# Performance work log

Hardware: AMD Instinct MI355X
Metric: run time of the kernel (lower is better)

The kernel has to match this reference:

```python
import jax, jax.numpy as jnp
import numpy as np

EPS = 1e-8
LN_EPS = 1e-5
DIM, NHEADS = 512, 8
HEAD_DIM = DIM // NHEADS
SCALE = HEAD_DIM ** -0.5
ROLE_VOCAB = 8


def _layernorm(x, g, b):
    mu = x.mean(-1, keepdims=True)
    var = ((x - mu) ** 2).mean(-1, keepdims=True)
    return (x - mu) * jax.lax.rsqrt(var + LN_EPS) * g + b


def setup_inputs() -> dict:
    key = jax.random.key(0)
    ks = jax.random.split(key, 16)
    B, K, L, D = 8, 4, 1024, DIM
    s = 1.0 / np.sqrt(D)
    return {
        "state_repr": jax.random.normal(ks[0], (B, K, L, D), jnp.float32),
        "residue_mask": jax.random.randint(ks[1], (B, K, L), 0, 2) > 0,
        "state_weights": jax.random.uniform(ks[2], (B, K), jnp.float32),
        "state_roles": jax.random.randint(ks[3], (B, K), 0, ROLE_VOCAB),
        "state_present_mask": jnp.ones((B, K), dtype=bool),
        "role_emb": jax.random.normal(ks[4], (ROLE_VOCAB, D), jnp.float32),
        "Wq": jax.random.normal(ks[5], (D, D), jnp.float32) * s,
        "Wk": jax.random.normal(ks[6], (D, D), jnp.float32) * s,
        "Wv": jax.random.normal(ks[7], (D, D), jnp.float32) * s,
        "Wo": jax.random.normal(ks[8], (D, D), jnp.float32) * s,
        "ln1_g": jnp.ones((3 * D,), jnp.float32),
        "ln1_b": jnp.zeros((3 * D,), jnp.float32),
        "Wg1": jax.random.normal(ks[9], (D, 3 * D), jnp.float32) / np.sqrt(3 * D),
        "bg1": jnp.zeros((D,), jnp.float32),
        "Wg2": jax.random.normal(ks[10], (D, D), jnp.float32) * s,
        "bg2": jnp.zeros((D,), jnp.float32),
        "norm_g": jnp.ones((D,), jnp.float32),
        "norm_b": jnp.zeros((D,), jnp.float32),
    }


def _forward(state_repr, residue_mask, state_weights, state_roles, state_present_mask,
             role_emb, Wq, Wk, Wv, Wo, ln1_g, ln1_b, Wg1, bg1, Wg2, bg2, norm_g, norm_b):
    B, K, L, D = state_repr.shape
    H, hd = NHEADS, HEAD_DIM
    roles = jnp.maximum(state_roles, 0)
    role_e = role_emb[roles][:, :, None, :]                       # [B,K,1,D]
    valid = residue_mask & state_present_mask[:, :, None]          # [B,K,L]

    # normalized state weights
    pres = state_present_mask.astype(jnp.float32)
    w = state_weights.astype(jnp.float32) * pres
    denom = w.sum(1, keepdims=True)
    fallback = pres / jnp.maximum(pres.sum(1, keepdims=True), 1.0)
    nsw = jnp.where(denom > EPS, w / jnp.maximum(denom, EPS), fallback)  # [B,K]

    x = (state_repr + role_e) * valid[..., None]
    x = x.transpose(0, 2, 1, 3)                                    # [B,L,K,D]
    valid_rlk = valid.transpose(0, 2, 1)                           # [B,L,K]

    def proj(W):  # torch Linear: y = x @ W.T
        return (x @ W.T).reshape(B, L, K, H, hd).transpose(0, 1, 3, 2, 4)  # [B,L,H,K,hd]

    q, k, v = proj(Wq), proj(Wk), proj(Wv)
    logits = jnp.einsum('blhqd,blhkd->blhqk', q, k) * SCALE
    logits = logits + jnp.log(jnp.maximum(nsw, EPS))[:, None, None, None, :]
    key_mask = valid_rlk[:, :, None, None, :]                      # [B,L,1,1,K]
    logits = jnp.where(key_mask, logits, -jnp.inf)
    attn = jax.nn.softmax(logits, axis=-1)
    attn = jnp.nan_to_num(attn, nan=0.0, posinf=0.0, neginf=0.0)
    attn_out = jnp.einsum('blhqk,blhkd->blhqd', attn, v)
    attn_out = attn_out.transpose(0, 1, 3, 2, 4).reshape(B, L, K, D)
    attn_out = (attn_out @ Wo.T) * valid_rlk[..., None]

    swr = nsw[:, None, :] * valid_rlk.astype(jnp.float32)          # [B,L,K]
    swr = swr / jnp.maximum(swr.sum(-1, keepdims=True), EPS)
    weighted_mean = jnp.sum(x * swr[..., None], axis=2)            # [B,L,D]
    attn_pooled = jnp.sum(attn_out * swr[..., None], axis=2)

    max_in = jnp.where(valid_rlk[..., None], x, -1e9)
    max_feat = max_in.max(axis=2)
    has_any = valid_rlk.any(axis=2, keepdims=True)
    max_feat = jnp.where(has_any, max_feat, 0.0)

    fusion_base = 0.5 * (attn_pooled + weighted_mean)
    gate_in = jnp.concatenate([attn_pooled, weighted_mean, max_feat], axis=-1)
    h = _layernorm(gate_in, ln1_g, ln1_b)
    h = jax.nn.gelu(h @ Wg1.T + bg1, approximate=False)
    gate = jax.nn.sigmoid(h @ Wg2.T + bg2)
    fused = gate * fusion_base + (1.0 - gate) * max_feat
    fused = _layernorm(fused + weighted_mean, norm_g, norm_b)

    attn_mean = attn.mean(axis=(2, 3))                             # [B,L,K]
    return fused, attn_pooled, weighted_mean, max_feat, attn_mean, nsw


def reference(state_repr, residue_mask, state_weights, state_roles, state_present_mask,
              role_emb, Wq, Wk, Wv, Wo, ln1_g, ln1_b, Wg1, bg1, Wg2, bg2, norm_g, norm_b):
    return _forward(state_repr, residue_mask, state_weights, state_roles, state_present_mask,
                    role_emb, Wq, Wk, Wv, Wo, ln1_g, ln1_b, Wg1, bg1, Wg2, bg2, norm_g, norm_b)
```

## Files before the change

kernel.cpp:

```cpp
#include <hip/hip_runtime.h>
#include <math.h>

#define BB 8
#define KK 4
#define LL 1024
#define DD 512
#define HD 64
#define D3 1536
#define MM (BB*LL*KK)
#define BL (BB*LL)
#define SCALE 0.125f
#define EPSF 1e-8f
#define LN_EPSF 1e-5f

typedef _Float16 hfrag __attribute__((ext_vector_type(8)));
typedef float f32x4 __attribute__((ext_vector_type(4)));

__device__ __forceinline__ unsigned short f2h(float f) {
    _Float16 h = (_Float16)f;
    unsigned short u; __builtin_memcpy(&u, &h, 2); return u;
}
__device__ __forceinline__ float h2f(unsigned short u) {
    _Float16 h; __builtin_memcpy(&h, &u, 2); return (float)h;
}

__device__ __forceinline__ void glds16(const unsigned short* g, unsigned short* l) {
    __builtin_amdgcn_global_load_lds(
        (const __attribute__((address_space(1))) void*)g,
        (__attribute__((address_space(3))) void*)l, 16, 0, 0);
}

__device__ __forceinline__ void nsw_compute(const float* sw, const int* pres,
                                            int b, float* nswv) {
    float w[KK], pr[KK]; float denom = 0.f, ps = 0.f;
    #pragma unroll
    for (int k = 0; k < KK; ++k) {
        pr[k] = pres[b*KK + k] ? 1.f : 0.f;
        w[k]  = sw[b*KK + k] * pr[k];
        denom += w[k]; ps += pr[k];
    }
    #pragma unroll
    for (int k = 0; k < KK; ++k)
        nswv[k] = (denom > EPSF) ? w[k] / fmaxf(denom, EPSF)
                                 : pr[k] / fmaxf(ps, 1.f);
}

#define WSZ 262144
#define OG1 1048576
#define OG2 1835008
#define WTOT 2097152
__global__ __launch_bounds__(256) void cvt_weights(
        const float* __restrict__ Wq, const float* __restrict__ Wk,
        const float* __restrict__ Wv, const float* __restrict__ Wo,
        const float* __restrict__ Wg1, const float* __restrict__ Wg2,
        unsigned short* __restrict__ dst) {
    int t = blockIdx.x * 256 + threadIdx.x;
    int e = t * 4;
    const float* src; int off;
    if      (e < WSZ)    { src = Wq;  off = e; }
    else if (e < 2*WSZ)  { src = Wk;  off = e - WSZ; }
    else if (e < 3*WSZ)  { src = Wv;  off = e - 2*WSZ; }
    else if (e < OG1)    { src = Wo;  off = e - 3*WSZ; }
    else if (e < OG2)    { src = Wg1; off = e - OG1; }
    else                 { src = Wg2; off = e - OG2; }
    float4 v = *(const float4*)(src + off);
    ushort4 o;
    o.x = f2h(v.x); o.y = f2h(v.y); o.z = f2h(v.z); o.w = f2h(v.w);
    *(ushort4*)(dst + e) = o;
}

__global__ __launch_bounds__(256) void buildx_kernel(
        const float* __restrict__ SR, const int* __restrict__ residue,
        const int* __restrict__ pres, const int* __restrict__ roles,
        const float* __restrict__ role_emb, const float* __restrict__ sw,
        unsigned short* __restrict__ Xh, float* __restrict__ rowmask,
        float* __restrict__ out_wm, float* __restrict__ out_mx,
        float* __restrict__ f_nsw) {
    int t  = blockIdx.x * 256 + threadIdx.x;
    int bl = t >> 7;
    int d4 = (t & 127) << 2;
    int b  = bl >> 10, l = bl & 1023;
    float nswv[KK];
    nsw_compute(sw, pres, b, nswv);
    float mk[KK], swr[KK];
    float ssum = 0.f, many = 0.f;
    #pragma unroll
    for (int k = 0; k < KK; ++k) {
        int bk = b*KK + k;
        bool valid = (residue[(size_t)bk*LL + l] != 0) && (pres[bk] != 0);
        mk[k]  = valid ? 1.f : 0.f;
        swr[k] = nswv[k] * mk[k];
        ssum += swr[k]; many += mk[k];
    }
    float inv = 1.f / fmaxf(ssum, EPSF);
    bool hasany = many > 0.5f;
    float wmx = 0.f, wmy = 0.f, wmz = 0.f, wmw = 0.f;
    float mxx = -1e9f, mxy = -1e9f, mxz = -1e9f, mxw = -1e9f;
    #pragma unroll
    for (int k = 0; k < KK; ++k) {
        int bk = b*KK + k;
        int role = roles[bk]; if (role < 0) role = 0;
        float4 sr = *(const float4*)(SR + ((size_t)bk*LL + l)*DD + d4);
        float4 re = *(const float4*)(role_emb + (size_t)role*DD + d4);
        float xx = (sr.x + re.x)*mk[k], xy = (sr.y + re.y)*mk[k];
        float xz = (sr.z + re.z)*mk[k], xw = (sr.w + re.w)*mk[k];
        ushort4 xs; xs.x = f2h(xx); xs.y = f2h(xy); xs.z = f2h(xz); xs.w = f2h(xw);
        *(ushort4*)(Xh + (size_t)(bl*KK + k)*DD + d4) = xs;
        float s = swr[k]*inv;
        wmx = fmaf(xx, s, wmx); wmy = fmaf(xy, s, wmy);
        wmz = fmaf(xz, s, wmz); wmw = fmaf(xw, s, wmw);
        if (mk[k] > 0.5f) {
            mxx = fmaxf(mxx, xx); mxy = fmaxf(mxy, xy);
            mxz = fmaxf(mxz, xz); mxw = fmaxf(mxw, xw);
        }
    }
    if (!hasany) { mxx = mxy = mxz = mxw = 0.f; }
    float4 wmv; wmv.x = wmx; wmv.y = wmy; wmv.z = wmz; wmv.w = wmw;
    float4 mxv; mxv.x = mxx; mxv.y = mxy; mxv.z = mxz; mxv.w = mxw;
    *(float4*)(out_wm + (size_t)bl*DD + d4) = wmv;
    *(float4*)(out_mx + (size_t)bl*DD + d4) = mxv;
    if (d4 == 0) {
        #pragma unroll
        for (int k = 0; k < KK; ++k) rowmask[bl*KK + k] = mk[k];
    }
    if (blockIdx.x == 0 && threadIdx.x < BB*KK) {
        int bb = threadIdx.x >> 2, kk2 = threadIdx.x & 3;
        float nv[KK];
        nsw_compute(sw, pres, bb, nv);
        f_nsw[threadIdx.x] = nv[kk2];
    }
}

template<int TM, int EPI, int OUTH, int QKVR, int SWZ>
__global__ __launch_bounds__(256) void gemm_mfma(
        const unsigned short* __restrict__ A, const unsigned short* __restrict__ W,
        void* __restrict__ Cv, int M, int N, int Kd,
        const float* __restrict__ bias, const float* __restrict__ rowmask) {
    constexpr int FI = TM / 32;
    __shared__ __align__(16) unsigned short As[TM*32];
    __shared__ __align__(16) unsigned short Bs[128*32];
    const int tid  = threadIdx.x;
    const int wave = tid >> 6, lane = tid & 63;
    int m0, n0;
    if (SWZ) {
        int id = blockIdx.x;
        int c = id & 7, j = id >> 3;
        int mloc = j / 12;
        m0 = (c*32 + mloc) * TM;
        n0 = (j - mloc*12) * 128;
    } else {
        m0 = blockIdx.y * TM; n0 = blockIdx.x * 128;
    }
    const int srow = lane >> 2;
    const int scol = (lane & 3) << 3;
    const int arow = (TM == 128) ? (wave*32 + srow)
                   : (TM == 64)  ? (wave*16 + srow)
                   :               ((wave & 1)*16 + srow);
    const bool astage = (TM >= 64) || (wave < 2);
    const unsigned short* Ag0 = A + (size_t)(m0 + arow) * Kd + scol;
    const unsigned short* Ag1 = Ag0 + (size_t)16 * Kd;
    unsigned short* Al0 = As + arow*32 + scol;
    unsigned short* Al1 = Al0 + 16*32;
    const unsigned short* Wp0 = W + (size_t)(n0 + wave*32 + srow) * Kd + scol;
    const unsigned short* Wp1 = Wp0 + (size_t)16 * Kd;
    unsigned short* Bl0 = Bs + (wave*32 + srow)*32 + scol;
    unsigned short* Bl1 = Bl0 + 16*32;
    const int wr = (wave >> 1) * (TM/2);
    const int wc = (wave & 1) * 64;
    const int fr = lane & 15;
    const int fq = (lane >> 4) * 8;
    f32x4 acc[FI][4] = {};
    for (int k0 = 0; k0 < Kd; k0 += 32) {
        if (astage)    glds16(Ag0 + k0, Al0);
        if (TM == 128) glds16(Ag1 + k0, Al1);
        glds16(Wp0 + k0, Bl0);
        glds16(Wp1 + k0, Bl1);
        __syncthreads();
        hfrag af[FI], bf[4];
        #pragma unroll
        for (int i = 0; i < FI; ++i)
            af[i] = *(const hfrag*)(As + (wr + i*16 + fr)*32 + fq);
        #pragma unroll
        for (int j = 0; j < 4; ++j)
            bf[j] = *(const hfrag*)(Bs + (wc + j*16 + fr)*32 + fq);
        #pragma unroll
        for (int i = 0; i < FI; ++i)
            #pragma unroll
            for (int j = 0; j < 4; ++j)
                acc[i][j] = __builtin_amdgcn_mfma_f32_16x16x32_f16(af[i], bf[j], acc[i][j], 0, 0, 0);
        __syncthreads();
    }
    unsigned short* Ch = (unsigned short*)Cv;
    int Nout = N, colbase = n0;
    if (QKVR) {
        const int seg = n0 >> 9;
        Ch = (unsigned short*)Cv + (size_t)seg * M * 512;
        Nout = 512;
        colbase = n0 - (seg << 9);
    }
    #pragma unroll
    for (int i = 0; i < FI; ++i) {
        const int row = m0 + wr + i*16 + (lane >> 4)*4;
        #pragma unroll
        for (int j = 0; j < 4; ++j) {
            const int col = colbase + wc + j*16 + (lane & 15);
            float bv = (EPI == 2) ? bias[col] : 0.f;
            #pragma unroll
            for (int r = 0; r < 4; ++r) {
                float v = acc[i][j][r];
                if (EPI == 2) { v += bv; v = 0.5f * v * (1.f + erff(v * 0.70710678118654752f)); }
                if (OUTH) Ch[(size_t)(row + r) * Nout + col] = f2h(v);
                else      ((float*)Cv)[(size_t)(row + r) * Nout + col] = v;
            }
        }
    }
}

__global__ __launch_bounds__(512, 2) void gemm_qkv_8p(
        const unsigned short* __restrict__ A, const unsigned short* __restrict__ W,
        unsigned short* __restrict__ Cbase) {
    __shared__ __align__(16) unsigned short smem[65536];
    const int tid  = threadIdx.x;
    const int wave = tid >> 6, lane = tid & 63;
    const int id = blockIdx.x;
    const int wg = (id & 7) * 96 + (id >> 3);
    const int m0 = (wg / 6) * 256;
    const int n0 = (wg % 6) * 256;
    const int wm = wave >> 2, wn = wave & 3;
    const int fr = lane & 15, q = lane >> 4;
    const int c0 = (wave << 6) | lane;
    const int r0 = c0 >> 2, cc0 = c0 & 3;
    const int c1 = c0 + 512;
    const int r1 = c1 >> 2, cc1 = c1 & 3;
    const unsigned short* Ag0 = A + (size_t)(m0 + r0)*512 + ((cc0 ^ ((r0 >> 1) & 3)) << 3);
    const unsigned short* Ag1 = A + (size_t)(m0 + r1)*512 + ((cc1 ^ ((r1 >> 1) & 3)) << 3);
    const unsigned short* Wp0 = W + (size_t)(n0 + r0)*512 + ((cc0 ^ ((r0 >> 1) & 3)) << 3);
    const unsigned short* Wp1 = W + (size_t)(n0 + r1)*512 + ((cc1 ^ ((r1 >> 1) & 3)) << 3);
    const int lA0 = c0 << 3, lA1 = c1 << 3;
    int aoff[8], boff[4];
    #pragma unroll
    for (int mf = 0; mf < 8; ++mf) {
        int row = (wm << 7) + (mf << 4) + fr;
        aoff[mf] = (row << 5) + ((q ^ ((row >> 1) & 3)) << 3);
    }
    #pragma unroll
    for (int nf = 0; nf < 4; ++nf) {
        int row = (wn << 6) + (nf << 4) + fr;
        boff[nf] = (row << 5) + ((q ^ ((row >> 1) & 3)) << 3);
    }
    f32x4 acc[8][4] = {};

#define VMWAIT(N) asm volatile("s_waitcnt vmcnt(" #N ")" ::: "memory")
#define STAGE(tt) do { unsigned short* _d = smem + (((tt) & 3) << 14); \
        const int _ko = (tt) << 5; \
        glds16(Ag0 + _ko, _d + lA0); glds16(Ag1 + _ko, _d + lA1); \
        glds16(Wp0 + _ko, _d + 8192 + lA0); glds16(Wp1 + _ko, _d + 8192 + lA1); } while (0)
#define MFROW(ai, areg) \
        acc[ai][0] = __builtin_amdgcn_mfma_f32_16x16x32_f16(areg, b0, acc[ai][0], 0, 0, 0); \
        acc[ai][1] = __builtin_amdgcn_mfma_f32_16x16x32_f16(areg, b1, acc[ai][1], 0, 0, 0); \
        acc[ai][2] = __builtin_amdgcn_mfma_f32_16x16x32_f16(areg, b2, acc[ai][2], 0, 0, 0); \
        acc[ai][3] = __builtin_amdgcn_mfma_f32_16x16x32_f16(areg, b3, acc[ai][3], 0, 0, 0);
#define TILE(t, STG, VM) do { \
        const unsigned short* _Ab = smem + (((t) & 3) << 14); \
        const unsigned short* _Bb = _Ab + 8192; \
        VMWAIT(VM); \
        __builtin_amdgcn_s_barrier(); \
        __builtin_amdgcn_sched_barrier(0); \
        hfrag b0 = *(const hfrag*)(_Bb + boff[0]); \
        hfrag b1 = *(const hfrag*)(_Bb + boff[1]); \
        hfrag b2 = *(const hfrag*)(_Bb + boff[2]); \
        hfrag b3 = *(const hfrag*)(_Bb + boff[3]); \
        hfrag a0_ = *(const hfrag*)(_Ab + aoff[0]); \
        hfrag a1_ = *(const hfrag*)(_Ab + aoff[1]); \
        hfrag a2_ = *(const hfrag*)(_Ab + aoff[2]); \
        hfrag a3_ = *(const hfrag*)(_Ab + aoff[3]); \
        hfrag a4_ = *(const hfrag*)(_Ab + aoff[4]); \
        hfrag a5_ = *(const hfrag*)(_Ab + aoff[5]); \
        hfrag a6_ = *(const hfrag*)(_Ab + aoff[6]); \
        hfrag a7_ = *(const hfrag*)(_Ab + aoff[7]); \
        if (STG) STAGE((t) + 3); \
        __builtin_amdgcn_s_setprio(1); \
        MFROW(0, a0_) MFROW(1, a1_) MFROW(2, a2_) MFROW(3, a3_) \
        MFROW(4, a4_) MFROW(5, a5_) MFROW(6, a6_) MFROW(7, a7_) \
        __builtin_amdgcn_s_setprio(0); \
    } while (0)

    STAGE(0); STAGE(1); STAGE(2);
    for (int t = 0; t < 13; ++t) TILE(t, 1, 8);
    TILE(13, 0, 8);
    TILE(14, 0, 4);
    TILE(15, 0, 0);
#undef TILE
#undef MFROW
#undef STAGE
#undef VMWAIT

    const int gc0 = n0 + (wn << 6);
    const int seg = gc0 >> 9;
    unsigned short* Cs = Cbase + (size_t)seg * ((size_t)MM * 512);
    const int cb = gc0 & 511;
    #pragma unroll
    for (int mf = 0; mf < 8; ++mf) {
        const int grow = m0 + (wm << 7) + (mf << 4) + (q << 2);
        #pragma unroll
        for (int nf = 0; nf < 4; ++nf) {
            const int col = cb + (nf << 4) + fr;
            #pragma unroll
            for (int r = 0; r < 4; ++r)
                Cs[(size_t)(grow + r) * 512 + col] = f2h(acc[mf][nf][r]);
        }
    }
}

__global__ __launch_bounds__(256) void wo_pool_kernel(
        const unsigned short* __restrict__ A,
        const unsigned short* __restrict__ W,
        const float* __restrict__ sw, const int* __restrict__ pres,
        const float* __restrict__ rmask,
        const float* __restrict__ in_wm, const float* __restrict__ in_mx,
        const float* __restrict__ ln1_g, const float* __restrict__ ln1_b,
        float* __restrict__ out_ap, unsigned short* __restrict__ hin) {
    __shared__ __align__(16) unsigned short As[32*32];
    __shared__ __align__(16) unsigned short Bs[512*32];
    const int tid = threadIdx.x, wave = tid >> 6, lane = tid & 63;
    const int m0 = blockIdx.x * 32;
    const int srow = lane >> 2, scol = (lane & 3) << 3;
    const unsigned short* Ag = A + (size_t)(m0 + wave*16 + srow)*512 + scol;
    unsigned short* Al = As + (wave*16 + srow)*32 + scol;
    const int brow = wave*128 + srow;
    const unsigned short* Wg = W + (size_t)brow*512 + scol;
    unsigned short* Blb = Bs + brow*32 + scol;
    const int q = lane >> 4, frl = lane & 15;
    const int fq = q * 8;
    f32x4 acc[2][8] = {};
    for (int k0 = 0; k0 < 512; k0 += 32) {
        if (wave < 2) glds16(Ag + k0, Al);
        #pragma unroll
        for (int i = 0; i < 8; ++i)
            glds16(Wg + (size_t)i*16*512 + k0, Blb + i*16*32);
        __syncthreads();
        hfrag af[2], bf[8];
        #pragma unroll
        for (int i = 0; i < 2; ++i)
            af[i] = *(const hfrag*)(As + (i*16 + frl)*32 + fq);
        #pragma unroll
        for (int j = 0; j < 8; ++j)
            bf[j] = *(const hfrag*)(Bs + (wave*128 + j*16 + frl)*32 + fq);
        #pragma unroll
        for (int i = 0; i < 2; ++i)
            #pragma unroll
            for (int j = 0; j < 8; ++j)
                acc[i][j] = __builtin_amdgcn_mfma_f32_16x16x32_f16(af[i], bf[j], acc[i][j], 0, 0, 0);
        __syncthreads();
    }
    float* ap_s = (float*)Bs;
    const int bl0 = m0 >> 2;
    const int b = bl0 >> 10;
    float nv[KK];
    nsw_compute(sw, pres, b, nv);
    #pragma unroll
    for (int i = 0; i < 2; ++i) {
        int bl_loc = i*4 + q;
        int blg = bl0 + bl_loc;
        float s4[KK]; float ssum = 0.f;
        #pragma unroll
        for (int k = 0; k < KK; ++k) { s4[k] = nv[k] * rmask[blg*4 + k]; ssum += s4[k]; }
        float inv = 1.f / fmaxf(ssum, EPSF);
        #pragma unroll
        for (int j = 0; j < 8; ++j) {
            float ap = 0.f;
            #pragma unroll
            for (int r = 0; r < KK; ++r) ap = fmaf(s4[r]*inv, acc[i][j][r], ap);
            ap_s[bl_loc*512 + wave*128 + j*16 + frl] = ap;
        }
    }
    __syncthreads();
    const int blq = tid >> 5;
    const int c0  = (tid & 31) * 16;
    const int blg = bl0 + blq;
    float4 ap4[4], wm4[4], mx4[4];
    #pragma unroll
    for (int v = 0; v < 4; ++v) {
        ap4[v] = *(const float4*)(ap_s + blq*512 + c0 + v*4);
        wm4[v] = *(const float4*)(in_wm + (size_t)blg*512 + c0 + v*4);
        mx4[v] = *(const float4*)(in_mx + (size_t)blg*512 + c0 + v*4);
    }
    float s = 0.f, s2 = 0.f;
    #pragma unroll
    for (int c = 0; c < 16; ++c) {
        float ap = ((const float*)ap4)[c];
        float wm = ((const float*)wm4)[c];
        float mx = ((const float*)mx4)[c];
        s += ap + wm + mx; s2 += ap*ap + wm*wm + mx*mx;
    }
    #pragma unroll
    for (int o = 1; o < 32; o <<= 1) {
        s  += __shfl_xor(s,  o, 32);
        s2 += __shfl_xor(s2, o, 32);
    }
    float mu = s * (1.f/(float)D3);
    float var = s2 * (1.f/(float)D3) - mu*mu;
    float rstd = rsqrtf(var + LN_EPSF);
    #pragma unroll
    for (int v = 0; v < 4; ++v)
        *(float4*)(out_ap + (size_t)blg*512 + c0 + v*4) = ap4[v];
    #pragma unroll
    for (int seg = 0; seg < 3; ++seg) {
        const float* src = (seg == 0) ? (const float*)ap4
                         : (seg == 1) ? (const float*)wm4 : (const float*)mx4;
        int gofs = seg*512 + c0;
        #pragma unroll
        for (int v = 0; v < 4; ++v) {
            float4 g4 = *(const float4*)(ln1_g + gofs + v*4);
            float4 b4 = *(const float4*)(ln1_b + gofs + v*4);
            ushort4 o;
            o.x = f2h((src[v*4+0]-mu)*rstd*g4.x + b4.x);
            o.y = f2h((src[v*4+1]-mu)*rstd*g4.y + b4.y);
            o.z = f2h((src[v*4+2]-mu)*rstd*g4.z + b4.z);
            o.w = f2h((src[v*4+3]-mu)*rstd*g4.w + b4.w);
            *(ushort4*)(hin + (size_t)blg*D3 + gofs + v*4) = o;
        }
    }
}

__global__ __launch_bounds__(256) void wg2_final_kernel(
        const unsigned short* __restrict__ A,
        const unsigned short* __restrict__ W,
        const float* __restrict__ bg2,
        const float* __restrict__ in_ap, const float* __restrict__ in_wm,
        const float* __restrict__ in_mx,
        const float* __restrict__ norm_g, const float* __restrict__ norm_b,
        float* __restrict__ fused) {
    __shared__ __align__(16) unsigned short As[16*32];
    __shared__ __align__(16) unsigned short Bs[512*32];
    __shared__ float rs[16*4], rq[16*4];
    const int tid = threadIdx.x, wave = tid >> 6, lane = tid & 63;
    const int m0 = blockIdx.x * 16;
    const int srow = lane >> 2, scol = (lane & 3) << 3;
    const unsigned short* Ag = A + (size_t)(m0 + srow)*512 + scol;
    unsigned short* Al = As + srow*32 + scol;
    const int brow = wave*128 + srow;
    const unsigned short* Wg = W + (size_t)brow*512 + scol;
    unsigned short* Blb = Bs + brow*32 + scol;
    const int q = lane >> 4, frl = lane & 15;
    const int fq = q * 8;
    f32x4 acc[8] = {};
    for (int k0 = 0; k0 < 512; k0 += 32) {
        if (wave == 0) glds16(Ag + k0, Al);
        #pragma unroll
        for (int i = 0; i < 8; ++i)
            glds16(Wg + (size_t)i*16*512 + k0, Blb + i*16*32);
        __syncthreads();
        hfrag af, bf[8];
        af = *(const hfrag*)(As + frl*32 + fq);
        #pragma unroll
        for (int j = 0; j < 8; ++j)
            bf[j] = *(const hfrag*)(Bs + (wave*128 + j*16 + frl)*32 + fq);
        #pragma unroll
        for (int j = 0; j < 8; ++j)
            acc[j] = __builtin_amdgcn_mfma_f32_16x16x32_f16(af, bf[j], acc[j], 0, 0, 0);
        __syncthreads();
    }
    float pre[8][4];
    float s[4] = {}, s2[4] = {};
    #pragma unroll
    for (int j = 0; j < 8; ++j) {
        int col = wave*128 + j*16 + frl;
        float bv = bg2[col];
        #pragma unroll
        for (int r = 0; r < 4; ++r) {
            int row = m0 + q*4 + r;
            float g = 1.f / (1.f + expf(-(acc[j][r] + bv)));
            float ap = in_ap[(size_t)row*512 + col];
            float wm = in_wm[(size_t)row*512 + col];
            float mx = in_mx[(size_t)row*512 + col];
            float p = g*0.5f*(ap + wm) + (1.f - g)*mx + wm;
            pre[j][r] = p;
            s[r] += p; s2[r] += p*p;
        }
    }
    #pragma unroll
    for (int r = 0; r < 4; ++r) {
        #pragma unroll
        for (int o = 1; o < 16; o <<= 1) {
            s[r]  += __shfl_xor(s[r],  o, 64);
            s2[r] += __shfl_xor(s2[r], o, 64);
        }
        if (frl == 0) {
            rs[(q*4+r)*4 + wave] = s[r];
            rq[(q*4+r)*4 + wave] = s2[r];
        }
    }
    __syncthreads();
    float mu[4], rstd[4];
    #pragma unroll
    for (int r = 0; r < 4; ++r) {
        int rl = q*4 + r;
        float ts  = rs[rl*4] + rs[rl*4+1] + rs[rl*4+2] + rs[rl*4+3];
        float tq  = rq[rl*4] + rq[rl*4+1] + rq[rl*4+2] + rq[rl*4+3];
        float m = ts * (1.f/(float)DD);
        float v = tq * (1.f/(float)DD) - m*m;
        mu[r] = m; rstd[r] = rsqrtf(v + LN_EPSF);
    }
    #pragma unroll
    for (int j = 0; j < 8; ++j) {
        int col = wave*128 + j*16 + frl;
        float g = norm_g[col], bb = norm_b[col];
        #pragma unroll
        for (int r = 0; r < 4; ++r) {
            int row = m0 + q*4 + r;
            fused[(size_t)row*512 + col] = (pre[j][r]-mu[r])*rstd[r]*g + bb;
        }
    }
}

__global__ __launch_bounds__(256) void attn_kernel(
        unsigned short* Qb ,
        const unsigned short* __restrict__ Kb, const unsigned short* __restrict__ Vb,
        const float* __restrict__ sw, const int* __restrict__ pres,
        const float* __restrict__ rowmask,
        float* __restrict__ attn_mean_out) {
    __shared__ float qs[KK][DD];
    __shared__ float ksm[KK][DD];
    __shared__ float vs[KK][DD];
    __shared__ float att[128];
    __shared__ float lw[KK], mk[KK];
    int bl = blockIdx.x, b = bl >> 10, mb = bl * KK;
    int tid = threadIdx.x;
    const ushort4* q4 = (const ushort4*)(Qb + (size_t)mb*DD);
    const ushort4* k4 = (const ushort4*)(Kb + (size_t)mb*DD);
    const ushort4* v4 = (const ushort4*)(Vb + (size_t)mb*DD);
    #pragma unroll
    for (int p = 0; p < 2; ++p) {
        int idx = p*256 + tid;
        int k = idx >> 7, dd = (idx & 127) << 2;
        ushort4 a = q4[idx];
        qs[k][dd] = h2f(a.x); qs[k][dd+1] = h2f(a.y); qs[k][dd+2] = h2f(a.z); qs[k][dd+3] = h2f(a.w);
        ushort4 c = k4[idx];
        ksm[k][dd] = h2f(c.x); ksm[k][dd+1] = h2f(c.y); ksm[k][dd+2] = h2f(c.z); ksm[k][dd+3] = h2f(c.w);
        ushort4 e = v4[idx];
        vs[k][dd] = h2f(e.x); vs[k][dd+1] = h2f(e.y); vs[k][dd+2] = h2f(e.z); vs[k][dd+3] = h2f(e.w);
    }
    if (tid < KK) {
        float nv[KK];
        nsw_compute(sw, pres, b, nv);
        lw[tid] = logf(fmaxf(nv[tid], EPSF));
        mk[tid] = rowmask[mb + tid];
    }
    __syncthreads();
    if (tid < 128) {
        int h = tid >> 4, i = (tid >> 2) & 3, j = tid & 3;
        float s = 0.f;
        #pragma unroll 16
        for (int d = 0; d < HD; ++d) s = fmaf(qs[i][h*HD + d], ksm[j][h*HD + d], s);
        float lg = s * SCALE + lw[j];
        att[tid] = (mk[j] > 0.5f) ? lg : -INFINITY;
    }
    __syncthreads();
    if (tid < 32) {
        int base = tid * 4;
        float l0 = att[base], l1 = att[base+1], l2 = att[base+2], l3 = att[base+3];
        float m = fmaxf(fmaxf(l0, l1), fmaxf(l2, l3));
        if (m == -INFINITY) {
            att[base] = att[base+1] = att[base+2] = att[base+3] = 0.f;
        } else {
            float e0 = expf(l0 - m), e1 = expf(l1 - m), e2 = expf(l2 - m), e3 = expf(l3 - m);
            float inv = 1.f / (e0 + e1 + e2 + e3);
            att[base] = e0*inv; att[base+1] = e1*inv; att[base+2] = e2*inv; att[base+3] = e3*inv;
        }
    }
    __syncthreads();
    if (tid < KK) {
        float s = 0.f;
        for (int hi = 0; hi < 32; ++hi) s += att[hi*4 + tid];
        attn_mean_out[(size_t)bl*KK + tid] = s * (1.f/32.f);
    }
    float outv[8];
    #pragma unroll
    for (int p = 0; p < 8; ++p) {
        int idx = p*256 + tid;
        int i = idx >> 9, dc = idx & 511, h = dc >> 6;
        float s = 0.f;
        #pragma unroll
        for (int j = 0; j < KK; ++j) s = fmaf(att[h*16 + i*4 + j], vs[j][dc], s);
        outv[p] = s;
    }
    #pragma unroll
    for (int p = 0; p < 8; ++p) {
        int idx = p*256 + tid;
        int i = idx >> 9, dc = idx & 511;
        Qb[(size_t)(mb+i)*DD + dc] = f2h(outv[p]);
    }
}

extern "C" void kernel_launch(void* const* d_in, const int* in_sizes, int n_in,
                              void* d_out, int out_size, void* d_ws, size_t ws_size,
                              hipStream_t stream) {
    const float* SR      = (const float*)d_in[0];
    const int*   residue = (const int*)d_in[1];
    const float* sw      = (const float*)d_in[2];
    const int*   roles   = (const int*)d_in[3];
    const int*   pres    = (const int*)d_in[4];
    const float* role_emb= (const float*)d_in[5];
    const float* Wq      = (const float*)d_in[6];
    const float* Wk      = (const float*)d_in[7];
    const float* Wv      = (const float*)d_in[8];
    const float* Wo      = (const float*)d_in[9];
    const float* ln1_g   = (const float*)d_in[10];
    const float* ln1_b   = (const float*)d_in[11];
    const float* Wg1     = (const float*)d_in[12];
    const float* bg1     = (const float*)d_in[13];
    const float* Wg2     = (const float*)d_in[14];
    const float* bg2     = (const float*)d_in[15];
    const float* norm_g  = (const float*)d_in[16];
    const float* norm_b  = (const float*)d_in[17];

    float* out = (float*)d_out;
    const size_t BLD = (size_t)BL * DD;
    float* f_fused = out;
    float* f_ap    = out + BLD;
    float* f_wm    = out + 2*BLD;
    float* f_mx    = out + 3*BLD;
    float* f_am    = out + 4*BLD;
    float* f_nsw   = out + 4*BLD + (size_t)BL*KK;

    char* base = (char*)d_ws;
    const size_t MD2 = (size_t)MM * DD * 2;
    unsigned short* Xh = (unsigned short*)(base);
    unsigned short* Qh = (unsigned short*)(base + MD2);
    unsigned short* Kh = (unsigned short*)(base + 2*MD2);
    unsigned short* Vh = (unsigned short*)(base + 3*MD2);
    unsigned short* Wb = (unsigned short*)(base + 4*MD2);
    float* rmask = (float*)(base + 4*MD2 + (size_t)WTOT*2);
    unsigned short* AOh  = Qh;
    unsigned short* Hin  = Vh;
    unsigned short* Hbuf = Xh;
    const unsigned short* Wqkv = Wb;
    const unsigned short* Woh  = Wb + 3*WSZ;
    const unsigned short* Wg1h = Wb + OG1;
    const unsigned short* Wg2h = Wb + OG2;

    dim3 blk(256);

    cvt_weights<<<WTOT/1024, blk, 0, stream>>>(Wq, Wk, Wv, Wo, Wg1, Wg2, Wb);
    buildx_kernel<<<(BL*128)/256, blk, 0, stream>>>(SR, residue, pres, roles, role_emb,
                                                    sw, Xh, rmask, f_wm, f_mx, f_nsw);

    gemm_qkv_8p<<<dim3(768), dim3(512), 0, stream>>>(Xh, Wqkv, Qh);

    attn_kernel<<<BL, blk, 0, stream>>>(Qh, Kh, Vh, sw, pres, rmask, f_am);

    wo_pool_kernel<<<dim3(MM/32), blk, 0, stream>>>(
        AOh, Woh, sw, pres, rmask, f_wm, f_mx, ln1_g, ln1_b, f_ap, Hin);

    gemm_mfma<32,2,1,0,0><<<dim3(4, BL/32), blk, 0, stream>>>(
        Hin, Wg1h, Hbuf, BL, DD, D3, bg1, nullptr);

    wg2_final_kernel<<<dim3(BL/16), blk, 0, stream>>>(
        Hbuf, Wg2h, bg2, f_ap, f_wm, f_mx, norm_g, norm_b, f_fused);
}
```

Baseline: 385.7 us.

## Shrink QKV GEMM tile to 256x128 with triple-buffered LDS for higher occupancy

The QKV projection GEMM tile goes from 256x256 to 256x128, with 8 waves arranged 4x2 and each wave holding a 64x64 accumulator. The LDS ring drops from four stages to three (72 KB) and the launch bound rises to 4 blocks per CU. The grid doubles to 1536 blocks. The goal is more resident waves and better latency hiding, at the cost of re-reading A more often and having less compute per loaded tile and a shallower prefetch.

```diff
diff --git a/kernel.cpp b/kernel.cpp
--- a/kernel.cpp
+++ b/kernel.cpp
@@ -216,31 +216,29 @@
     }
 }
 
-__global__ __launch_bounds__(512, 2) void gemm_qkv_8p(
+__global__ __launch_bounds__(512, 4) void gemm_qkv_8p(
         const unsigned short* __restrict__ A, const unsigned short* __restrict__ W,
         unsigned short* __restrict__ Cbase) {
-    __shared__ __align__(16) unsigned short smem[65536];
+    __shared__ __align__(16) unsigned short smem[36864];
     const int tid  = threadIdx.x;
     const int wave = tid >> 6, lane = tid & 63;
     const int id = blockIdx.x;
-    const int wg = (id & 7) * 96 + (id >> 3);
-    const int m0 = (wg / 6) * 256;
-    const int n0 = (wg % 6) * 256;
-    const int wm = wave >> 2, wn = wave & 3;
+    const int wg = (id & 7) * 192 + (id >> 3);
+    const int m0 = (wg / 12) * 256;
+    const int n0 = (wg % 12) * 128;
+    const int wm = wave >> 1, wn = wave & 1;
     const int fr = lane & 15, q = lane >> 4;
-    const int c0 = (wave << 6) | lane;
-    const int r0 = c0 >> 2, cc0 = c0 & 3;
-    const int c1 = c0 + 512;
-    const int r1 = c1 >> 2, cc1 = c1 & 3;
-    const unsigned short* Ag0 = A + (size_t)(m0 + r0)*512 + ((cc0 ^ ((r0 >> 1) & 3)) << 3);
-    const unsigned short* Ag1 = A + (size_t)(m0 + r1)*512 + ((cc1 ^ ((r1 >> 1) & 3)) << 3);
-    const unsigned short* Wp0 = W + (size_t)(n0 + r0)*512 + ((cc0 ^ ((r0 >> 1) & 3)) << 3);
-    const unsigned short* Wp1 = W + (size_t)(n0 + r1)*512 + ((cc1 ^ ((r1 >> 1) & 3)) << 3);
-    const int lA0 = c0 << 3, lA1 = c1 << 3;
-    int aoff[8], boff[4];
-    #pragma unroll
-    for (int mf = 0; mf < 8; ++mf) {
-        int row = (wm << 7) + (mf << 4) + fr;
+    const int srow = tid >> 2, scc = tid & 3;
+    const int sswz = (scc ^ ((srow >> 1) & 3)) << 3;
+    const unsigned short* Ag0 = A + (size_t)(m0 + srow)*512 + sswz;
+    const unsigned short* Ag1 = Ag0 + (size_t)128*512;
+    const unsigned short* Wg0 = W + (size_t)(n0 + srow)*512 + sswz;
+    const int lA0 = tid << 3;
+    const int lA1 = (tid + 512) << 3;
+    int aoff[4], boff[4];
+    #pragma unroll
+    for (int mf = 0; mf < 4; ++mf) {
+        int row = (wm << 6) + (mf << 4) + fr;
         aoff[mf] = (row << 5) + ((q ^ ((row >> 1) & 3)) << 3);
     }
     #pragma unroll
@@ -248,20 +246,20 @@
         int row = (wn << 6) + (nf << 4) + fr;
         boff[nf] = (row << 5) + ((q ^ ((row >> 1) & 3)) << 3);
     }
-    f32x4 acc[8][4] = {};
+    f32x4 acc[4][4] = {};
 
 #define VMWAIT(N) asm volatile("s_waitcnt vmcnt(" #N ")" ::: "memory")
-#define STAGE(tt) do { unsigned short* _d = smem + (((tt) & 3) << 14); \
+#define STAGE(tt) do { unsigned short* _d = smem + ((tt) % 3) * 12288; \
         const int _ko = (tt) << 5; \
         glds16(Ag0 + _ko, _d + lA0); glds16(Ag1 + _ko, _d + lA1); \
-        glds16(Wp0 + _ko, _d + 8192 + lA0); glds16(Wp1 + _ko, _d + 8192 + lA1); } while (0)
+        glds16(Wg0 + _ko, _d + 8192 + lA0); } while (0)
 #define MFROW(ai, areg) \
         acc[ai][0] = __builtin_amdgcn_mfma_f32_16x16x32_f16(areg, b0, acc[ai][0], 0, 0, 0); \
         acc[ai][1] = __builtin_amdgcn_mfma_f32_16x16x32_f16(areg, b1, acc[ai][1], 0, 0, 0); \
         acc[ai][2] = __builtin_amdgcn_mfma_f32_16x16x32_f16(areg, b2, acc[ai][2], 0, 0, 0); \
         acc[ai][3] = __builtin_amdgcn_mfma_f32_16x16x32_f16(areg, b3, acc[ai][3], 0, 0, 0);
 #define TILE(t, STG, VM) do { \
-        const unsigned short* _Ab = smem + (((t) & 3) << 14); \
+        const unsigned short* _Ab = smem + ((t) % 3) * 12288; \
         const unsigned short* _Bb = _Ab + 8192; \
         VMWAIT(VM); \
         __builtin_amdgcn_s_barrier(); \
@@ -274,21 +272,16 @@
         hfrag a1_ = *(const hfrag*)(_Ab + aoff[1]); \
         hfrag a2_ = *(const hfrag*)(_Ab + aoff[2]); \
         hfrag a3_ = *(const hfrag*)(_Ab + aoff[3]); \
-        hfrag a4_ = *(const hfrag*)(_Ab + aoff[4]); \
-        hfrag a5_ = *(const hfrag*)(_Ab + aoff[5]); \
-        hfrag a6_ = *(const hfrag*)(_Ab + aoff[6]); \
-        hfrag a7_ = *(const hfrag*)(_Ab + aoff[7]); \
-        if (STG) STAGE((t) + 3); \
+        if (STG) STAGE((t) + 2); \
         __builtin_amdgcn_s_setprio(1); \
         MFROW(0, a0_) MFROW(1, a1_) MFROW(2, a2_) MFROW(3, a3_) \
-        MFROW(4, a4_) MFROW(5, a5_) MFROW(6, a6_) MFROW(7, a7_) \
         __builtin_amdgcn_s_setprio(0); \
     } while (0)
 
-    STAGE(0); STAGE(1); STAGE(2);
-    for (int t = 0; t < 13; ++t) TILE(t, 1, 8);
-    TILE(13, 0, 8);
-    TILE(14, 0, 4);
+    STAGE(0); STAGE(1);
+    #pragma unroll
+    for (int t = 0; t < 14; ++t) TILE(t, 1, 3);
+    TILE(14, 0, 3);
     TILE(15, 0, 0);
 #undef TILE
 #undef MFROW
@@ -300,8 +293,8 @@
     unsigned short* Cs = Cbase + (size_t)seg * ((size_t)MM * 512);
     const int cb = gc0 & 511;
     #pragma unroll
-    for (int mf = 0; mf < 8; ++mf) {
-        const int grow = m0 + (wm << 7) + (mf << 4) + (q << 2);
+    for (int mf = 0; mf < 4; ++mf) {
+        const int grow = m0 + (wm << 6) + (mf << 4) + (q << 2);
         #pragma unroll
         for (int nf = 0; nf < 4; ++nf) {
             const int col = cb + (nf << 4) + fr;
@@ -646,7 +639,7 @@
     buildx_kernel<<<(BL*128)/256, blk, 0, stream>>>(SR, residue, pres, roles, role_emb,
                                                     sw, Xh, rmask, f_wm, f_mx, f_nsw);
 
-    gemm_qkv_8p<<<dim3(768), dim3(512), 0, stream>>>(Xh, Wqkv, Qh);
+    gemm_qkv_8p<<<dim3(1536), dim3(512), 0, stream>>>(Xh, Wqkv, Qh);
 
     attn_kernel<<<BL, blk, 0, stream>>>(Qh, Kh, Vh, sw, pres, rmask, f_am);
 
```

Result: faster. 375.2 us (-2.7%).
